# Kernel optimization log

Hardware: AMD Instinct MI355X
Metric: run time of the kernel (lower is better)

Reference implementation:

```python
import jax, jax.numpy as jnp
import numpy as np

B, Hg, Wg, K, D, SD = 4, 128, 128, 16, 256, 64
N = Hg * Wg
MGAT_R0 = 1.5
TV_W = 1e-3
BIG_NEG = -10000.0
LN_EPS = 1e-5
# (r, s0, sl, cb) per geodesic scale
SCALES = ((1.5, 0.25, 0.2, 0.7), (2.5, 0.35, 0.2, 0.5), (4.0, 0.55, 0.25, 0.3))


def _build_grid_knn(H, W, Kn):
    # K nearest grid offsets (incl. self), deterministic tie-break
    cand = [(dy, dx) for dy in range(-3, 4) for dx in range(-3, 4)]
    cand.sort(key=lambda o: (o[0] * o[0] + o[1] * o[1], o[0], o[1]))
    offs = np.array(cand[:Kn])                                  # (K,2)
    ii, jj = np.meshgrid(np.arange(H), np.arange(W), indexing='ij')
    pos = np.stack([ii.ravel(), jj.ravel()], -1)                # (N,2)
    nb = pos[:, None, :] + offs[None]                           # (N,K,2)
    nb[..., 0] = np.clip(nb[..., 0], 0, H - 1)
    nb[..., 1] = np.clip(nb[..., 1], 0, W - 1)
    idx = (nb[..., 0] * W + nb[..., 1]).astype(np.int32)        # (N,K)
    rel = (nb - pos[:, None, :]).astype(np.float32)             # (N,K,2)
    geod = np.sqrt((rel ** 2).sum(-1)).astype(np.float32)       # (N,K)
    rel = rel / np.clip(np.abs(rel).max(axis=(0, 1), keepdims=True), 1e-6, None)
    return idx, rel, geod


def _lin(key, fan_in, fan_out):
    kw, kb = jax.random.split(key)
    s = 1.0 / np.sqrt(fan_in)
    return (jax.random.uniform(kw, (fan_in, fan_out), jnp.float32, -s, s),
            jax.random.uniform(kb, (fan_out,), jnp.float32, -s, s))


def setup_inputs() -> dict:
    key = jax.random.key(0)
    ks = jax.random.split(key, 14)
    idx, rel, geod = _build_grid_knn(Hg, Wg, K)
    inp = {
        'z': jax.random.normal(ks[0], (B, N, D), jnp.float32),
        'S': jax.random.normal(ks[1], (B, N, SD), jnp.float32),
        'rel': jnp.asarray(rel), 'geod': jnp.asarray(geod), 'idx': jnp.asarray(idx),
    }
    inp['Wq'], inp['bq'] = _lin(ks[2], D, D)
    inp['Wk'], inp['bk'] = _lin(ks[3], D, D)
    inp['Wv'], inp['bv'] = _lin(ks[4], D, D)
    inp['Wo'], inp['bo'] = _lin(ks[5], D, D)
    inp['ln_g'] = jnp.ones((D,), jnp.float32)
    inp['ln_b'] = jnp.zeros((D,), jnp.float32)
    inp['Ws1'], inp['bs1'] = _lin(ks[6], 2, 16)
    inp['Ws2'], inp['bs2'] = _lin(ks[7], 16, 16)
    inp['Wzg'], inp['bzg'] = _lin(ks[8], D, 16)
    inp['Wph'], inp['bph'] = _lin(ks[9], 32, 3)
    inp['Wsg'], inp['bsg'] = _lin(ks[10], 32, 3)
    return inp


def _forward(z, S, rel, geod, Wq, bq, Wk, bk, Wv, bv, Wo, bo, ln_g, ln_b,
             Ws1, bs1, Ws2, bs2, Wzg, bzg, Wph, bph, Wsg, bsg, idx):
    gelu = lambda x: jax.nn.gelu(x, approximate=False)
    q = z @ Wq + bq
    k = z @ Wk + bk
    v = z @ Wv + bv
    kN = k[:, idx]                                   # (B,N,K,D) neighbor gather
    vN = v[:, idx]                                   # (B,N,K,D)
    S_n = S[:, idx]                                  # (B,N,K,SD)
    m1 = S.mean(-1, keepdims=True)
    m2 = (S * S).mean(-1, keepdims=True)
    s_emb = gelu(gelu(jnp.concatenate([m1, m2], -1) @ Ws1 + bs1) @ Ws2 + bs2)
    z_emb = gelu(z @ Wzg + bzg)
    ker_in = jnp.concatenate([s_emb, z_emb], -1)     # (B,N,32)
    abc = ker_in @ Wph + bph                         # (B,N,3)
    La = jnp.exp(abc[..., 0]); Lb = abc[..., 1]; Lc = jnp.exp(abc[..., 2])
    # A = L L^T with L = [[La,0],[Lb,Lc]] -> symmetric 2x2 per node
    A00 = La * La; A01 = La * Lb; A11 = Lb * Lb + Lc * Lc   # (B,N)
    r0 = rel[None, ..., 0]; r1 = rel[None, ..., 1]          # (1,N,K)
    rAr = (A00[..., None] * r0 * r0 + 2.0 * A01[..., None] * r0 * r1
           + A11[..., None] * r1 * r1)                      # (B,N,K)
    sim = jnp.einsum('bns,bnks->bnk', S, S_n)
    content = jnp.einsum('bnd,bnkd->bnk', q, kN) / np.sqrt(D).astype(np.float32)
    g = jax.nn.softmax(ker_in @ Wsg + bsg, axis=-1)         # (B,N,3)
    geod_b = geod[None]                                     # (1,N,K)
    center_prior = jnp.exp(-geod_b ** 2 / MGAT_R0 ** 2)
    att_logits = jnp.zeros_like(content)
    for i, (r, s0, sl, cb) in enumerate(SCALES):
        hard_mask = (geod > r).astype(z.dtype)[None]
        sigma2 = jnp.maximum((s0 + sl * geod_b) ** 2, 1e-6)
        att_i = (content - rAr / sigma2 - 0.25 * geod_b + 1.0 * sim
                 + cb * center_prior + hard_mask * BIG_NEG)
        att_logits = att_logits + att_i * g[..., i:i + 1]
    att = jax.nn.softmax(att_logits, axis=-1)               # (B,N,K)
    agg = jnp.einsum('bnk,bnkd->bnd', att, vN)
    h = z + (agg @ Wo + bo)                                 # dropout/drop_path = identity (eval)
    mu = h.mean(-1, keepdims=True)
    var = ((h - mu) ** 2).mean(-1, keepdims=True)
    out = ln_g * (h - mu) / jnp.sqrt(var + LN_EPS) + ln_b
    # TV regularizer on Frobenius norm of A over the HxW grid
    A_norm = jnp.sqrt(A00 * A00 + 2.0 * A01 * A01 + A11 * A11).reshape(B, Hg, Wg)
    dy = jnp.abs(A_norm[:, 1:, :] - A_norm[:, :-1, :]).mean()
    dx = jnp.abs(A_norm[:, :, 1:] - A_norm[:, :, :-1]).mean()
    reg = TV_W * (dx + dy)
    return out, reg


def reference(z, S, rel, geod, idx, Wq, bq, Wk, bk, Wv, bv, Wo, bo, ln_g, ln_b,
              Ws1, bs1, Ws2, bs2, Wzg, bzg, Wph, bph, Wsg, bsg):
    return _forward(z, S, rel, geod, Wq, bq, Wk, bk, Wv, bv, Wo, bo, ln_g, ln_b,
                    Ws1, bs1, Ws2, bs2, Wzg, bzg, Wph, bph, Wsg, bsg, idx)
```

## Files before the change

### kernel.cpp

```cpp
#include <hip/hip_runtime.h>
#include <hip/hip_bf16.h>
#include <math.h>


typedef unsigned short u16;
typedef unsigned int u32;
typedef __attribute__((ext_vector_type(8))) short short8;
typedef __attribute__((ext_vector_type(4))) float f32x4;

#define NB 16384
#define NROWS 65536
#define DD 256
#define SDD 64

__device__ __forceinline__ float b2f(u16 u) {
  union { unsigned int i; float f; } c; c.i = ((unsigned int)u) << 16; return c.f;
}
__device__ __forceinline__ float blo(unsigned int u) {
  union { unsigned int i; float f; } c; c.i = u << 16; return c.f;
}
__device__ __forceinline__ float bhi(unsigned int u) {
  union { unsigned int i; float f; } c; c.i = u & 0xFFFF0000u; return c.f;
}
__device__ __forceinline__ u16 f2b(float f) {
  union { float f; unsigned int i; } c; c.f = f;
  unsigned int i = c.i;
  return (u16)((i + 0x7FFFu + ((i >> 16) & 1u)) >> 16);
}
__device__ __forceinline__ float gelu_exact(float x) {
  return 0.5f * x * (1.0f + erff(x * 0.70710678118654752f));
}
__device__ __forceinline__ void gll16(const u16* g, u16* l) {
  __builtin_amdgcn_global_load_lds(
      (const __attribute__((address_space(1))) void*)g,
      (__attribute__((address_space(3))) void*)l, 16, 0, 0);
}
__device__ __forceinline__ u32 qsc(u32 w) {
  float lo = __uint_as_float(w << 16) * 0.0625f;
  float hi = __uint_as_float(w & 0xFFFF0000u) * 0.0625f;
  return (__float_as_uint(lo) >> 16) | (__float_as_uint(hi) & 0xFFFF0000u);
}

__global__ __launch_bounds__(256) void k_prep_w(
    const float* __restrict__ Wq, const float* __restrict__ Wk,
    const float* __restrict__ Wv, const float* __restrict__ Wo,
    const float* __restrict__ Wzg,
    const float* __restrict__ bq, const float* __restrict__ bk,
    const float* __restrict__ bv, const float* __restrict__ bzg,
    u16* __restrict__ WqkvT, u16* __restrict__ WoT, float* __restrict__ biasq)
{
  int gid = blockIdx.x * 256 + threadIdx.x;
  int stride = gridDim.x * 256;
  for (int e = gid; e < 229376; e += stride) {
    int j = e >> 8, kk = e & 255;
    float v;
    if (j < 256)      v = Wq[kk * 256 + j];
    else if (j < 512) v = Wk[kk * 256 + (j - 256)];
    else if (j < 768) v = Wv[kk * 256 + (j - 512)];
    else if (j < 784) v = Wzg[kk * 16 + (j - 768)];
    else              v = 0.0f;
    WqkvT[e] = f2b(v);
  }
  for (int e = gid; e < 65536; e += stride) {
    int j = e >> 8, kk = e & 255;
    WoT[e] = f2b(Wo[kk * 256 + j]);
  }
  for (int e = gid; e < 784; e += stride)
    biasq[e] = e < 256 ? bq[e] : e < 512 ? bk[e - 256]
             : e < 768 ? bv[e - 512] : bzg[e - 768];
}

__global__ __launch_bounds__(256) void k_pre(
    const float* __restrict__ z, const float* __restrict__ S,
    u16* __restrict__ zb, float* __restrict__ rowdat)
{
  int w = threadIdx.x >> 6, t = threadIdx.x & 63;
  int r = blockIdx.x * 4 + w;
  float4 zv = *(const float4*)(z + (size_t)r * DD + t * 4);
  *(ushort4*)(zb + (size_t)r * DD + t * 4) =
      make_ushort4(f2b(zv.x), f2b(zv.y), f2b(zv.z), f2b(zv.w));
  float sv = S[(size_t)r * SDD + t];
  float s1 = sv, s2 = sv * sv;
  #pragma unroll
  for (int o = 32; o; o >>= 1) { s1 += __shfl_xor(s1, o); s2 += __shfl_xor(s2, o); }
  if (t == 0) {
    rowdat[(size_t)r * 8 + 0] = s1 * (1.0f / 64.0f);
    rowdat[(size_t)r * 8 + 1] = s2 * (1.0f / 64.0f);
  }
}

__global__ __launch_bounds__(256) void k_mfma_qkv(
    const u16* __restrict__ A, const u16* __restrict__ BT,
    const float* __restrict__ biasq,
    u16* __restrict__ qb, u16* __restrict__ kb, u16* __restrict__ vb,
    float* __restrict__ ze)
{
  __shared__ u16 As[128 * 64];
  __shared__ u16 Bs[128 * 64];
  int t = threadIdx.x, wv = t >> 6, lane = t & 63;
  int m0 = blockIdx.x * 128, j0 = blockIdx.y * 128;
  int wm = (wv & 1) * 64, wn = (wv >> 1) * 64;
  int quad = lane >> 4, l15 = lane & 15;
  int srow = lane >> 3, scol = (lane & 7) * 8;
  f32x4 acc[4][4] = {};
  for (int kc = 0; kc < 256; kc += 64) {
    if (kc) __syncthreads();
    for (int it = 0; it < 4; ++it) {
      int c = it * 4 + wv;
      gll16(A + (size_t)(m0 + c * 8 + srow) * 256 + kc + scol, As + c * 512);
      gll16(BT + (size_t)(j0 + c * 8 + srow) * 256 + kc + scol, Bs + c * 512);
    }
    __syncthreads();
    #pragma unroll
    for (int ks = 0; ks < 64; ks += 32) {
      short8 af[4], bfr[4];
      #pragma unroll
      for (int mi = 0; mi < 4; ++mi)
        af[mi] = *(const short8*)&As[(wm + mi * 16 + l15) * 64 + ks + quad * 8];
      #pragma unroll
      for (int ni = 0; ni < 4; ++ni)
        bfr[ni] = *(const short8*)&Bs[(wn + ni * 16 + l15) * 64 + ks + quad * 8];
      #pragma unroll
      for (int mi = 0; mi < 4; ++mi)
        #pragma unroll
        for (int ni = 0; ni < 4; ++ni)
          acc[mi][ni] = __builtin_amdgcn_mfma_f32_16x16x32_bf16(
              af[mi], bfr[ni], acc[mi][ni], 0, 0, 0);
    }
  }
  if (j0 < 768) {
    u16* obuf = (j0 < 256) ? qb : (j0 < 512) ? kb : vb;
    int jb = j0 & 255;
    #pragma unroll
    for (int ni = 0; ni < 4; ++ni) {
      int gcol = j0 + wn + ni * 16 + l15;
      float bia = biasq[gcol];
      int colb = jb + wn + ni * 16 + l15;
      #pragma unroll
      for (int mi = 0; mi < 4; ++mi) {
        int grow = m0 + wm + mi * 16 + quad * 4;
        #pragma unroll
        for (int r = 0; r < 4; ++r)
          obuf[(size_t)(grow + r) * 256 + colb] = f2b(acc[mi][ni][r] + bia);
      }
    }
  } else if (wn == 0) {
    float bia = biasq[768 + l15];
    #pragma unroll
    for (int mi = 0; mi < 4; ++mi) {
      int grow = m0 + wm + mi * 16 + quad * 4;
      #pragma unroll
      for (int r = 0; r < 4; ++r)
        ze[(size_t)(grow + r) * 16 + l15] = gelu_exact(acc[mi][0][r] + bia);
    }
  }
}

__global__ __launch_bounds__(256) void k_post(
    const float* __restrict__ ze,
    const float* __restrict__ Ws1, const float* __restrict__ bs1,
    const float* __restrict__ Ws2, const float* __restrict__ bs2,
    const float* __restrict__ Wph, const float* __restrict__ bph,
    const float* __restrict__ Wsg, const float* __restrict__ bsg,
    float* __restrict__ rowdat)
{
  __shared__ float h1s[16][17];
  __shared__ float kin[16][33];
  __shared__ float abcs[16][8];
  int rloc = threadIdx.x >> 4, j = threadIdx.x & 15;
  int r = blockIdx.x * 16 + rloc;
  float m1 = rowdat[(size_t)r * 8 + 0];
  float m2 = rowdat[(size_t)r * 8 + 1];
  h1s[rloc][j] = gelu_exact(m1 * Ws1[j] + m2 * Ws1[16 + j] + bs1[j]);
  __syncthreads();
  float h2 = bs2[j];
  #pragma unroll
  for (int i = 0; i < 16; ++i) h2 += h1s[rloc][i] * Ws2[i * 16 + j];
  kin[rloc][j] = gelu_exact(h2);
  kin[rloc][16 + j] = ze[(size_t)r * 16 + j];
  __syncthreads();
  if (j < 6) {
    int c = j % 3;
    const float* Wp = (j < 3) ? Wph : Wsg;
    const float* bp = (j < 3) ? bph : bsg;
    float a = bp[c];
    #pragma unroll
    for (int i = 0; i < 32; ++i) a += kin[rloc][i] * Wp[i * 3 + c];
    abcs[rloc][j] = a;
  }
  __syncthreads();
  if (j == 0) {
    float La = expf(abcs[rloc][0]), Lb = abcs[rloc][1], Lc = expf(abcs[rloc][2]);
    float A00 = La * La, A01 = La * Lb, A11 = Lb * Lb + Lc * Lc;
    float g0 = abcs[rloc][3], g1 = abcs[rloc][4], g2 = abcs[rloc][5];
    float gm = fmaxf(g0, fmaxf(g1, g2));
    float e0 = expf(g0 - gm), e1 = expf(g1 - gm), e2 = expf(g2 - gm);
    float inv = 1.0f / (e0 + e1 + e2);
    float* rd = rowdat + (size_t)r * 8;
    rd[0] = A00; rd[1] = A01; rd[2] = A11;
    rd[3] = e0 * inv; rd[4] = e1 * inv; rd[5] = e2 * inv;
    rd[6] = sqrtf(A00 * A00 + 2.0f * A01 * A01 + A11 * A11);
  }
}

#define DYP 0x1004220331132212ULL
#define DXP 0x0312402313123122ULL

__global__ __launch_bounds__(256) void k_attn_mfma(
    const u16* __restrict__ q, const u16* __restrict__ k,
    const u16* __restrict__ v, const float* __restrict__ S,
    const float* __restrict__ rowdat, u16* __restrict__ aggp)
{
  __shared__ u16 KV[18432];
  __shared__ u16 Qs[16 * 264];
  __shared__ u16 Shi[64 * 72];
  __shared__ u16 Slo[64 * 72];
  __shared__ float scores[16 * 68];
  __shared__ float attf[16 * 68];
  __shared__ u16 attb[16 * 72];
  __shared__ float rds[16 * 8];

  int tid = threadIdx.x;
  int bid = blockIdx.x;
  int gidx = (bid & 7) * 512 + (bid >> 3);
  int b = gidx >> 10;
  int gid = gidx & 1023;
  int gy0 = (gid >> 5) << 2, gx0 = (gid & 31) << 2;
  int by0 = gy0 - 2; by0 = by0 < 0 ? 0 : (by0 > 120 ? 120 : by0);
  int bx0 = gx0 - 2; bx0 = bx0 < 0 ? 0 : (bx0 > 120 ? 120 : bx0);
  int oy = gy0 - by0, ox = gx0 - bx0;
  size_t bbase = (size_t)b << 14;

  int vpp = tid & 31, vdc = tid >> 5;
  size_t vn0 = bbase + (size_t)(by0 + (vpp >> 2)) * 128 + bx0 + ((vpp & 3) * 2);
  const u16* v0 = v + vn0 * 256;
  uint4 va[4], vb4[4];
  #pragma unroll
  for (int i = 0; i < 4; ++i) {
    va[i]  = *(const uint4*)(v0 + (vdc + i * 8) * 8);
    vb4[i] = *(const uint4*)(v0 + 256 + (vdc + i * 8) * 8);
  }

  {
    int rr8 = tid >> 5, cc = tid & 31;
    #pragma unroll
    for (int p = 0; p < 8; ++p) {
      size_t n = bbase + (size_t)(by0 + p) * 128 + bx0 + rr8;
      uint4 ld = *(const uint4*)(k + n * 256 + cc * 8);
      *(uint4*)&KV[(p * 8 + rr8) * 264 + cc * 8] = ld;
    }
    #pragma unroll
    for (int p = 0; p < 2; ++p) {
      int r = p * 8 + rr8;
      size_t n = bbase + (size_t)(gy0 + (r >> 2)) * 128 + gx0 + (r & 3);
      uint4 ld = *(const uint4*)(q + n * 256 + cc * 8);
      uint4 o;
      o.x = qsc(ld.x); o.y = qsc(ld.y); o.z = qsc(ld.z); o.w = qsc(ld.w);
      *(uint4*)&Qs[r * 264 + cc * 8] = o;
    }
  }
  {
    int u = tid >> 2, qq = tid & 3;
    size_t n = bbase + (size_t)(by0 + (u >> 3)) * 128 + bx0 + (u & 7);
    const float* srow = S + n * 64 + qq * 16;
    u32 hw[8], lw[8];
    #pragma unroll
    for (int i = 0; i < 4; ++i) {
      float4 s4 = *(const float4*)(srow + i * 4);
      u32 bx_ = __float_as_uint(s4.x), by_ = __float_as_uint(s4.y);
      u32 bz_ = __float_as_uint(s4.z), bw_ = __float_as_uint(s4.w);
      u32 hx = bx_ & 0xFFFF0000u, hy = by_ & 0xFFFF0000u;
      u32 hz = bz_ & 0xFFFF0000u, hww = bw_ & 0xFFFF0000u;
      hw[i * 2]     = (bx_ >> 16) | hy;
      hw[i * 2 + 1] = (bz_ >> 16) | hww;
      lw[i * 2]     = (__float_as_uint(s4.x - __uint_as_float(hx)) >> 16)
                    | (__float_as_uint(s4.y - __uint_as_float(hy)) & 0xFFFF0000u);
      lw[i * 2 + 1] = (__float_as_uint(s4.z - __uint_as_float(hz)) >> 16)
                    | (__float_as_uint(s4.w - __uint_as_float(hww)) & 0xFFFF0000u);
    }
    *(uint4*)&Shi[u * 72 + qq * 16]     = make_uint4(hw[0], hw[1], hw[2], hw[3]);
    *(uint4*)&Shi[u * 72 + qq * 16 + 8] = make_uint4(hw[4], hw[5], hw[6], hw[7]);
    *(uint4*)&Slo[u * 72 + qq * 16]     = make_uint4(lw[0], lw[1], lw[2], lw[3]);
    *(uint4*)&Slo[u * 72 + qq * 16 + 8] = make_uint4(lw[4], lw[5], lw[6], lw[7]);
  }
  if (tid < 128) {
    int r = tid >> 3, sl = tid & 7;
    size_t n = bbase + (size_t)(gy0 + (r >> 2)) * 128 + gx0 + (r & 3);
    rds[tid] = rowdat[n * 8 + sl];
  }
  for (int i = tid; i < 16 * 68; i += 256) attf[i] = 0.0f;
  __syncthreads();

  int w = tid >> 6, lane = tid & 63, l15 = lane & 15, quad = lane >> 4;

  {
    f32x4 acc = {0.f, 0.f, 0.f, 0.f};
    int arow = l15 * 264 + quad * 8;
    int brow = (w * 16 + l15) * 264 + quad * 8;
    #pragma unroll
    for (int ks = 0; ks < 8; ++ks) {
      short8 a  = *(const short8*)&Qs[arow + ks * 32];
      short8 bq = *(const short8*)&KV[brow + ks * 32];
      acc = __builtin_amdgcn_mfma_f32_16x16x32_bf16(a, bq, acc, 0, 0, 0);
    }
    int ucq = ((l15 >> 2) + oy) * 8 + (l15 & 3) + ox;
    int sa = ucq * 72 + quad * 8;
    int sb = (w * 16 + l15) * 72 + quad * 8;
    #pragma unroll
    for (int ks = 0; ks < 2; ++ks) {
      short8 ah = *(const short8*)&Shi[sa + ks * 32];
      short8 al = *(const short8*)&Slo[sa + ks * 32];
      short8 bh = *(const short8*)&Shi[sb + ks * 32];
      short8 bl = *(const short8*)&Slo[sb + ks * 32];
      acc = __builtin_amdgcn_mfma_f32_16x16x32_bf16(ah, bh, acc, 0, 0, 0);
      acc = __builtin_amdgcn_mfma_f32_16x16x32_bf16(ah, bl, acc, 0, 0, 0);
      acc = __builtin_amdgcn_mfma_f32_16x16x32_bf16(al, bh, acc, 0, 0, 0);
    }
    #pragma unroll
    for (int r4 = 0; r4 < 4; ++r4)
      scores[(quad * 4 + r4) * 68 + w * 16 + l15] = acc[r4];
  }
  __syncthreads();

  {
    int r = tid >> 4, g = tid & 15;
    int gy = gy0 + (r >> 2), gx = gx0 + (r & 3);
    int dy = (int)((DYP >> (g * 4)) & 15) - 2;
    int dx = (int)((DXP >> (g * 4)) & 15) - 2;
    int ny = gy + dy; ny = ny < 0 ? 0 : (ny > 127 ? 127 : ny);
    int nx = gx + dx; nx = nx < 0 ? 0 : (nx > 127 ? 127 : nx);
    int cdy = ny - gy, cdx = nx - gx;
    int u = (ny - by0) * 8 + (nx - bx0);
    float sc = scores[r * 68 + u];
    const float* rd = &rds[r * 8];
    float A00 = rd[0], A01 = rd[1], A11 = rd[2];
    float g0 = rd[3], g1 = rd[4], g2 = rd[5];
    float r0 = cdy * 0.5f, r1 = cdx * 0.5f;
    int ig2 = cdy * cdy + cdx * cdx;
    float ge2 = (float)ig2;
    float ge = sqrtf(ge2);
    float rAr = A00 * r0 * r0 + 2.0f * A01 * r0 * r1 + A11 * r1 * r1;
    float prior = __expf(-ge2 * (1.0f / 2.25f));
    float lg = sc - 0.25f * ge;
    { float s = 0.25f + 0.2f  * ge; float s2 = fmaxf(s * s, 1e-6f);
      lg += g0 * (-rAr * __builtin_amdgcn_rcpf(s2) + 0.7f * prior
                  + (ig2 >= 3  ? -10000.0f : 0.0f)); }
    { float s = 0.35f + 0.2f  * ge; float s2 = fmaxf(s * s, 1e-6f);
      lg += g1 * (-rAr * __builtin_amdgcn_rcpf(s2) + 0.5f * prior
                  + (ig2 >= 7  ? -10000.0f : 0.0f)); }
    { float s = 0.55f + 0.25f * ge; float s2 = fmaxf(s * s, 1e-6f);
      lg += g2 * (-rAr * __builtin_amdgcn_rcpf(s2) + 0.3f * prior
                  + (ig2 >= 17 ? -10000.0f : 0.0f)); }
    float m = lg;
    m = fmaxf(m, __shfl_xor(m, 1));
    m = fmaxf(m, __shfl_xor(m, 2));
    m = fmaxf(m, __shfl_xor(m, 4));
    m = fmaxf(m, __shfl_xor(m, 8));
    float e = __expf(lg - m);
    float sm = e;
    sm += __shfl_xor(sm, 1); sm += __shfl_xor(sm, 2);
    sm += __shfl_xor(sm, 4); sm += __shfl_xor(sm, 8);
    float att = e * __builtin_amdgcn_rcpf(sm);
    atomicAdd(&attf[r * 68 + u], att);
  }
  __syncthreads();

  {
    int r = tid >> 4, c4 = (tid & 15) * 4;
    float4 fv = *(const float4*)&attf[r * 68 + c4];
    u32 w0 = (u32)f2b(fv.x) | ((u32)f2b(fv.y) << 16);
    u32 w1 = (u32)f2b(fv.z) | ((u32)f2b(fv.w) << 16);
    *(uint2*)&attb[r * 72 + c4] = make_uint2(w0, w1);
  }
  {
    u32* VTw = (u32*)KV;
    #pragma unroll
    for (int i = 0; i < 4; ++i) {
      int d0 = (vdc + i * 8) * 8;
      u32 a0 = va[i].x, a1 = va[i].y, a2 = va[i].z, a3 = va[i].w;
      u32 b0 = vb4[i].x, b1 = vb4[i].y, b2 = vb4[i].z, b3 = vb4[i].w;
      VTw[(d0 + 0) * 36 + vpp] = (a0 & 0xFFFFu) | (b0 << 16);
      VTw[(d0 + 1) * 36 + vpp] = (a0 >> 16)     | (b0 & 0xFFFF0000u);
      VTw[(d0 + 2) * 36 + vpp] = (a1 & 0xFFFFu) | (b1 << 16);
      VTw[(d0 + 3) * 36 + vpp] = (a1 >> 16)     | (b1 & 0xFFFF0000u);
      VTw[(d0 + 4) * 36 + vpp] = (a2 & 0xFFFFu) | (b2 << 16);
      VTw[(d0 + 5) * 36 + vpp] = (a2 >> 16)     | (b2 & 0xFFFF0000u);
      VTw[(d0 + 6) * 36 + vpp] = (a3 & 0xFFFFu) | (b3 << 16);
      VTw[(d0 + 7) * 36 + vpp] = (a3 >> 16)     | (b3 & 0xFFFF0000u);
    }
  }
  __syncthreads();

  {
    short8 a0 = *(const short8*)&attb[l15 * 72 + quad * 8];
    short8 a1 = *(const short8*)&attb[l15 * 72 + 32 + quad * 8];
    #pragma unroll
    for (int ni = 0; ni < 4; ++ni) {
      int d = w * 64 + ni * 16 + l15;
      f32x4 ag = {0.f, 0.f, 0.f, 0.f};
      short8 bv0 = *(const short8*)&KV[d * 72 + quad * 8];
      short8 bv1 = *(const short8*)&KV[d * 72 + 32 + quad * 8];
      ag = __builtin_amdgcn_mfma_f32_16x16x32_bf16(a0, bv0, ag, 0, 0, 0);
      ag = __builtin_amdgcn_mfma_f32_16x16x32_bf16(a1, bv1, ag, 0, 0, 0);
      #pragma unroll
      for (int r4 = 0; r4 < 4; ++r4) {
        int row = quad * 4 + r4;
        size_t n = bbase + (size_t)(gy0 + (row >> 2)) * 128 + gx0 + (row & 3);
        aggp[n * 256 + d] = f2b(ag[r4]);
      }
    }
  }
}

__global__ __launch_bounds__(256) void k_mfma_out_ln(
    const u16* __restrict__ A, const u16* __restrict__ BT,
    const float* __restrict__ bo, const float* __restrict__ zres,
    const float* __restrict__ lng, const float* __restrict__ lnb,
    float* __restrict__ outp)
{
  __shared__ u16 As[128 * 64];
  __shared__ u16 Bs[256 * 64];
  int t = threadIdx.x, wv = t >> 6, lane = t & 63;
  int m0 = blockIdx.x * 128;
  int wm = wv * 32;
  int quad = lane >> 4, l15 = lane & 15;
  int srow = lane >> 3, scol = (lane & 7) * 8;
  f32x4 acc[2][16] = {};
  for (int kc = 0; kc < 256; kc += 64) {
    if (kc) __syncthreads();
    #pragma unroll
    for (int it = 0; it < 4; ++it) {
      int c = it * 4 + wv;
      gll16(A + (size_t)(m0 + c * 8 + srow) * 256 + kc + scol, As + c * 512);
    }
    #pragma unroll
    for (int it = 0; it < 8; ++it) {
      int c = it * 4 + wv;
      gll16(BT + (size_t)(c * 8 + srow) * 256 + kc + scol, Bs + c * 512);
    }
    __syncthreads();
    #pragma unroll
    for (int ks = 0; ks < 64; ks += 32) {
      short8 af[2], bfr[16];
      #pragma unroll
      for (int mi = 0; mi < 2; ++mi)
        af[mi] = *(const short8*)&As[(wm + mi * 16 + l15) * 64 + ks + quad * 8];
      #pragma unroll
      for (int ni = 0; ni < 16; ++ni)
        bfr[ni] = *(const short8*)&Bs[(ni * 16 + l15) * 64 + ks + quad * 8];
      #pragma unroll
      for (int mi = 0; mi < 2; ++mi)
        #pragma unroll
        for (int ni = 0; ni < 16; ++ni)
          acc[mi][ni] = __builtin_amdgcn_mfma_f32_16x16x32_bf16(
              af[mi], bfr[ni], acc[mi][ni], 0, 0, 0);
    }
  }
  float lg_[16], lb_[16], bo_[16];
  #pragma unroll
  for (int ni = 0; ni < 16; ++ni) {
    int col = ni * 16 + l15;
    lg_[ni] = lng[col]; lb_[ni] = lnb[col]; bo_[ni] = bo[col];
  }
  #pragma unroll
  for (int mi = 0; mi < 2; ++mi) {
    #pragma unroll
    for (int rr = 0; rr < 4; ++rr) {
      int row = m0 + wm + mi * 16 + quad * 4 + rr;
      float x[16];
      float s = 0.0f, sq = 0.0f;
      #pragma unroll
      for (int ni = 0; ni < 16; ++ni) {
        int col = ni * 16 + l15;
        float v = acc[mi][ni][rr] + bo_[ni] + zres[(size_t)row * 256 + col];
        x[ni] = v; s += v; sq += v * v;
      }
      #pragma unroll
      for (int o = 1; o < 16; o <<= 1) {
        s += __shfl_xor(s, o);
        sq += __shfl_xor(sq, o);
      }
      float mu = s * (1.0f / 256.0f);
      float var = sq * (1.0f / 256.0f) - mu * mu;
      float rstd = rsqrtf(var + 1e-5f);
      #pragma unroll
      for (int ni = 0; ni < 16; ++ni) {
        int col = ni * 16 + l15;
        outp[(size_t)row * 256 + col] = lg_[ni] * (x[ni] - mu) * rstd + lb_[ni];
      }
    }
  }
}

__global__ __launch_bounds__(256) void k_tv(
    const float* __restrict__ rowdat, float* __restrict__ sums)
{
  int gid = blockIdx.x * blockDim.x + threadIdx.x;
  int stride = gridDim.x * blockDim.x;
  float dy = 0.0f, dx = 0.0f;
  for (int e = gid; e < 4 * 127 * 128; e += stride) {
    int bb = e / 16256; int rem = e % 16256;
    int i = rem >> 7; int jj = rem & 127;
    int base = bb * 16384 + i * 128 + jj;
    dy += fabsf(rowdat[(size_t)(base + 128) * 8 + 6] - rowdat[(size_t)base * 8 + 6]);
  }
  for (int e = gid; e < 4 * 128 * 127; e += stride) {
    int bb = e / 16256; int rem = e % 16256;
    int i = rem / 127; int jj = rem % 127;
    int base = bb * 16384 + i * 128 + jj;
    dx += fabsf(rowdat[(size_t)(base + 1) * 8 + 6] - rowdat[(size_t)base * 8 + 6]);
  }
  #pragma unroll
  for (int o = 32; o; o >>= 1) { dy += __shfl_down(dy, o); dx += __shfl_down(dx, o); }
  if ((threadIdx.x & 63) == 0) {
    atomicAdd(&sums[0], dy);
    atomicAdd(&sums[1], dx);
  }
}

__global__ void k_reg(const float* __restrict__ sums, float* __restrict__ out)
{
  if (threadIdx.x == 0 && blockIdx.x == 0) {
    out[16777216] = 0.001f * (sums[0] + sums[1]) * (1.0f / 65024.0f);
  }
}

extern "C" void kernel_launch(void* const* d_in, const int* in_sizes, int n_in,
                              void* d_out, int out_size, void* d_ws, size_t ws_size,
                              hipStream_t stream)
{
  const float* z    = (const float*)d_in[0];
  const float* S    = (const float*)d_in[1];
  const float* rel  = (const float*)d_in[2];
  const float* geod = (const float*)d_in[3];
  const int*   idx  = (const int*)d_in[4];
  const float* Wq = (const float*)d_in[5];  const float* bq = (const float*)d_in[6];
  const float* Wk = (const float*)d_in[7];  const float* bk = (const float*)d_in[8];
  const float* Wv = (const float*)d_in[9];  const float* bv = (const float*)d_in[10];
  const float* Wo = (const float*)d_in[11]; const float* bo = (const float*)d_in[12];
  const float* lng = (const float*)d_in[13]; const float* lnb = (const float*)d_in[14];
  const float* Ws1 = (const float*)d_in[15]; const float* bs1 = (const float*)d_in[16];
  const float* Ws2 = (const float*)d_in[17]; const float* bs2 = (const float*)d_in[18];
  const float* Wzg = (const float*)d_in[19]; const float* bzg = (const float*)d_in[20];
  const float* Wph = (const float*)d_in[21]; const float* bph = (const float*)d_in[22];
  const float* Wsg = (const float*)d_in[23]; const float* bsg = (const float*)d_in[24];
  (void)rel; (void)geod; (void)idx;

  char* ws = (char*)d_ws;
  u16* zb = (u16*)ws;  ws += 33554432;
  u16* qb = (u16*)ws;  ws += 33554432;
  u16* kb = (u16*)ws;  ws += 33554432;
  u16* vb = (u16*)ws;  ws += 33554432;
  u16* WqkvT = (u16*)ws; ws += 458752;
  u16* WoT   = (u16*)ws; ws += 131072;
  float* biasq = (float*)ws; ws += 3136;
  float* ze    = (float*)ws; ws += 4194304;
  float* rowdat = (float*)ws; ws += 2097152;
  float* sums   = (float*)ws;
  u16* ab = zb;

  float* outp = (float*)d_out;

  hipMemsetAsync(sums, 0, 8, stream);
  k_prep_w<<<256, 256, 0, stream>>>(Wq, Wk, Wv, Wo, Wzg, bq, bk, bv, bzg,
                                    WqkvT, WoT, biasq);
  k_pre<<<NROWS / 4, 256, 0, stream>>>(z, S, zb, rowdat);
  k_mfma_qkv<<<dim3(512, 7), 256, 0, stream>>>(zb, WqkvT, biasq, qb, kb, vb, ze);
  k_post<<<NROWS / 16, 256, 0, stream>>>(ze, Ws1, bs1, Ws2, bs2,
                                         Wph, bph, Wsg, bsg, rowdat);
  k_attn_mfma<<<4096, 256, 0, stream>>>(qb, kb, vb, S, rowdat, ab);
  k_mfma_out_ln<<<512, 256, 0, stream>>>(ab, WoT, bo, z, lng, lnb, outp);
  k_tv<<<256, 256, 0, stream>>>(rowdat, sums);
  k_reg<<<1, 64, 0, stream>>>(sums, outp);
}
```

Before: 376.3 us.

## Fuse z bf16 conversion into QKV GEMM with resident A tile and LDS swizzle

The fp32 to bf16 conversion of z moves out of k_pre and into the QKV GEMM. Each block now converts its 128-row z tile once into a full-K LDS buffer and loops over all 7 column tiles, instead of launching 7 column blocks that each reload A. This drops the zb round trip through global memory and the repeated A loads. XOR swizzling is also added to the LDS layouts of both GEMMs to reduce bank conflicts. In exchange the grid shrinks to 512 blocks with 80KB of LDS each, which lowers occupancy and parallelism.

```diff
diff --git a/kernel.cpp b/kernel.cpp
--- a/kernel.cpp
+++ b/kernel.cpp
@@ -71,14 +71,10 @@
 }
 
 __global__ __launch_bounds__(256) void k_pre(
-    const float* __restrict__ z, const float* __restrict__ S,
-    u16* __restrict__ zb, float* __restrict__ rowdat)
+    const float* __restrict__ S, float* __restrict__ rowdat)
 {
   int w = threadIdx.x >> 6, t = threadIdx.x & 63;
   int r = blockIdx.x * 4 + w;
-  float4 zv = *(const float4*)(z + (size_t)r * DD + t * 4);
-  *(ushort4*)(zb + (size_t)r * DD + t * 4) =
-      make_ushort4(f2b(zv.x), f2b(zv.y), f2b(zv.z), f2b(zv.w));
   float sv = S[(size_t)r * SDD + t];
   float s1 = sv, s2 = sv * sv;
   #pragma unroll
@@ -90,68 +86,95 @@
 }
 
 __global__ __launch_bounds__(256) void k_mfma_qkv(
-    const u16* __restrict__ A, const u16* __restrict__ BT,
+    const float* __restrict__ z, const u16* __restrict__ BT,
     const float* __restrict__ biasq,
     u16* __restrict__ qb, u16* __restrict__ kb, u16* __restrict__ vb,
     float* __restrict__ ze)
 {
-  __shared__ u16 As[128 * 64];
+  __shared__ u16 As[128 * 256];
   __shared__ u16 Bs[128 * 64];
   int t = threadIdx.x, wv = t >> 6, lane = t & 63;
-  int m0 = blockIdx.x * 128, j0 = blockIdx.y * 128;
+  int m0 = blockIdx.x * 128;
   int wm = (wv & 1) * 64, wn = (wv >> 1) * 64;
   int quad = lane >> 4, l15 = lane & 15;
-  int srow = lane >> 3, scol = (lane & 7) * 8;
-  f32x4 acc[4][4] = {};
-  for (int kc = 0; kc < 256; kc += 64) {
-    if (kc) __syncthreads();
-    for (int it = 0; it < 4; ++it) {
-      int c = it * 4 + wv;
-      gll16(A + (size_t)(m0 + c * 8 + srow) * 256 + kc + scol, As + c * 512);
-      gll16(BT + (size_t)(j0 + c * 8 + srow) * 256 + kc + scol, Bs + c * 512);
-    }
-    __syncthreads();
-    #pragma unroll
-    for (int ks = 0; ks < 64; ks += 32) {
-      short8 af[4], bfr[4];
-      #pragma unroll
-      for (int mi = 0; mi < 4; ++mi)
-        af[mi] = *(const short8*)&As[(wm + mi * 16 + l15) * 64 + ks + quad * 8];
-      #pragma unroll
-      for (int ni = 0; ni < 4; ++ni)
-        bfr[ni] = *(const short8*)&Bs[(wn + ni * 16 + l15) * 64 + ks + quad * 8];
-      #pragma unroll
-      for (int mi = 0; mi < 4; ++mi)
+  int x7 = l15 & 7;
+  int srow = lane >> 3;
+  int scolsw = ((lane & 7) ^ (srow & 7)) << 3;
+
+  {
+    const float* zt = z + (size_t)m0 * 256;
+    #pragma unroll 8
+    for (int it = 0; it < 32; ++it) {
+      int idx = it * 256 + t;
+      int row = idx >> 6, g4 = idx & 63;
+      float4 v4 = *(const float4*)(zt + row * 256 + g4 * 4);
+      u32 w0 = (u32)f2b(v4.x) | ((u32)f2b(v4.y) << 16);
+      u32 w1 = (u32)f2b(v4.z) | ((u32)f2b(v4.w) << 16);
+      int slot = g4 >> 1, half = g4 & 1;
+      *(uint2*)&As[row * 256 + (((slot ^ (row & 7)) << 3) + (half << 2))] =
+          make_uint2(w0, w1);
+    }
+  }
+
+  for (int jt = 0; jt < 7; ++jt) {
+    int j0 = jt * 128;
+    f32x4 acc[4][4] = {};
+    for (int kc = 0; kc < 256; kc += 64) {
+      __syncthreads();
+      #pragma unroll
+      for (int it = 0; it < 4; ++it) {
+        int c = it * 4 + wv;
+        gll16(BT + (size_t)(j0 + c * 8 + srow) * 256 + kc + scolsw, Bs + c * 512);
+      }
+      __syncthreads();
+      #pragma unroll
+      for (int ks = 0; ks < 64; ks += 32) {
+        short8 af[4], bfr[4];
+        int sl = (ks >> 3) + quad;
         #pragma unroll
-        for (int ni = 0; ni < 4; ++ni)
-          acc[mi][ni] = __builtin_amdgcn_mfma_f32_16x16x32_bf16(
-              af[mi], bfr[ni], acc[mi][ni], 0, 0, 0);
-    }
-  }
-  if (j0 < 768) {
-    u16* obuf = (j0 < 256) ? qb : (j0 < 512) ? kb : vb;
-    int jb = j0 & 255;
-    #pragma unroll
-    for (int ni = 0; ni < 4; ++ni) {
-      int gcol = j0 + wn + ni * 16 + l15;
-      float bia = biasq[gcol];
-      int colb = jb + wn + ni * 16 + l15;
+        for (int mi = 0; mi < 4; ++mi) {
+          int row = wm + mi * 16 + l15;
+          int slot = (kc + ks + quad * 8) >> 3;
+          af[mi] = *(const short8*)&As[row * 256 + ((slot ^ x7) << 3)];
+        }
+        #pragma unroll
+        for (int ni = 0; ni < 4; ++ni) {
+          int row = wn + ni * 16 + l15;
+          bfr[ni] = *(const short8*)&Bs[row * 64 + ((sl ^ x7) << 3)];
+        }
+        #pragma unroll
+        for (int mi = 0; mi < 4; ++mi)
+          #pragma unroll
+          for (int ni = 0; ni < 4; ++ni)
+            acc[mi][ni] = __builtin_amdgcn_mfma_f32_16x16x32_bf16(
+                af[mi], bfr[ni], acc[mi][ni], 0, 0, 0);
+      }
+    }
+    if (j0 < 768) {
+      u16* obuf = (j0 < 256) ? qb : (j0 < 512) ? kb : vb;
+      int jb = j0 & 255;
+      #pragma unroll
+      for (int ni = 0; ni < 4; ++ni) {
+        int gcol = j0 + wn + ni * 16 + l15;
+        float bia = biasq[gcol];
+        int colb = jb + wn + ni * 16 + l15;
+        #pragma unroll
+        for (int mi = 0; mi < 4; ++mi) {
+          int grow = m0 + wm + mi * 16 + quad * 4;
+          #pragma unroll
+          for (int r = 0; r < 4; ++r)
+            obuf[(size_t)(grow + r) * 256 + colb] = f2b(acc[mi][ni][r] + bia);
+        }
+      }
+    } else if (wn == 0) {
+      float bia = biasq[768 + l15];
       #pragma unroll
       for (int mi = 0; mi < 4; ++mi) {
         int grow = m0 + wm + mi * 16 + quad * 4;
         #pragma unroll
         for (int r = 0; r < 4; ++r)
-          obuf[(size_t)(grow + r) * 256 + colb] = f2b(acc[mi][ni][r] + bia);
-      }
-    }
-  } else if (wn == 0) {
-    float bia = biasq[768 + l15];
-    #pragma unroll
-    for (int mi = 0; mi < 4; ++mi) {
-      int grow = m0 + wm + mi * 16 + quad * 4;
-      #pragma unroll
-      for (int r = 0; r < 4; ++r)
-        ze[(size_t)(grow + r) * 16 + l15] = gelu_exact(acc[mi][0][r] + bia);
+          ze[(size_t)(grow + r) * 16 + l15] = gelu_exact(acc[mi][0][r] + bia);
+      }
     }
   }
 }
@@ -424,30 +447,33 @@
   int m0 = blockIdx.x * 128;
   int wm = wv * 32;
   int quad = lane >> 4, l15 = lane & 15;
-  int srow = lane >> 3, scol = (lane & 7) * 8;
+  int x7 = l15 & 7;
+  int srow = lane >> 3;
+  int scolsw = ((lane & 7) ^ (srow & 7)) << 3;
   f32x4 acc[2][16] = {};
   for (int kc = 0; kc < 256; kc += 64) {
     if (kc) __syncthreads();
     #pragma unroll
     for (int it = 0; it < 4; ++it) {
       int c = it * 4 + wv;
-      gll16(A + (size_t)(m0 + c * 8 + srow) * 256 + kc + scol, As + c * 512);
+      gll16(A + (size_t)(m0 + c * 8 + srow) * 256 + kc + scolsw, As + c * 512);
     }
     #pragma unroll
     for (int it = 0; it < 8; ++it) {
       int c = it * 4 + wv;
-      gll16(BT + (size_t)(c * 8 + srow) * 256 + kc + scol, Bs + c * 512);
+      gll16(BT + (size_t)(c * 8 + srow) * 256 + kc + scolsw, Bs + c * 512);
     }
     __syncthreads();
     #pragma unroll
     for (int ks = 0; ks < 64; ks += 32) {
       short8 af[2], bfr[16];
+      int sl = (ks >> 3) + quad;
       #pragma unroll
       for (int mi = 0; mi < 2; ++mi)
-        af[mi] = *(const short8*)&As[(wm + mi * 16 + l15) * 64 + ks + quad * 8];
+        af[mi] = *(const short8*)&As[(wm + mi * 16 + l15) * 64 + ((sl ^ x7) << 3)];
       #pragma unroll
       for (int ni = 0; ni < 16; ++ni)
-        bfr[ni] = *(const short8*)&Bs[(ni * 16 + l15) * 64 + ks + quad * 8];
+        bfr[ni] = *(const short8*)&Bs[(ni * 16 + l15) * 64 + ((sl ^ x7) << 3)];
       #pragma unroll
       for (int mi = 0; mi < 2; ++mi)
         #pragma unroll
@@ -547,7 +573,7 @@
   (void)rel; (void)geod; (void)idx;
 
   char* ws = (char*)d_ws;
-  u16* zb = (u16*)ws;  ws += 33554432;
+  u16* ab = (u16*)ws;  ws += 33554432;
   u16* qb = (u16*)ws;  ws += 33554432;
   u16* kb = (u16*)ws;  ws += 33554432;
   u16* vb = (u16*)ws;  ws += 33554432;
@@ -557,15 +583,14 @@
   float* ze    = (float*)ws; ws += 4194304;
   float* rowdat = (float*)ws; ws += 2097152;
   float* sums   = (float*)ws;
-  u16* ab = zb;
 
   float* outp = (float*)d_out;
 
   hipMemsetAsync(sums, 0, 8, stream);
   k_prep_w<<<256, 256, 0, stream>>>(Wq, Wk, Wv, Wo, Wzg, bq, bk, bv, bzg,
                                     WqkvT, WoT, biasq);
-  k_pre<<<NROWS / 4, 256, 0, stream>>>(z, S, zb, rowdat);
-  k_mfma_qkv<<<dim3(512, 7), 256, 0, stream>>>(zb, WqkvT, biasq, qb, kb, vb, ze);
+  k_pre<<<NROWS / 4, 256, 0, stream>>>(S, rowdat);
+  k_mfma_qkv<<<512, 256, 0, stream>>>(z, WqkvT, biasq, qb, kb, vb, ze);
   k_post<<<NROWS / 16, 256, 0, stream>>>(ze, Ws1, bs1, Ws2, bs2,
                                          Wph, bph, Wsg, bsg, rowdat);
   k_attn_mfma<<<4096, 256, 0, stream>>>(qb, kb, vb, S, rowdat, ab);
```

Measured after the change: 396.0 us. 5.3% more time.
